# Kernel tuning notes

Hardware: AMD Instinct MI355X
Metric: run time of the kernel (lower is better)

## Reference

```python
import jax, jax.numpy as jnp
import numpy as np
from jax import lax

C, H, W = 1024, 128, 128
N = 4096
SIZE_RATIO = 8.0
ITERS = 10
INIT_LAMBDA = 0.01
MIN_LAMBDA = 1e-6
MAX_LAMBDA = 100.0


def to_homogeneous(x):
    return jnp.concatenate([x, jnp.ones(x.shape[:-1] + (1,), x.dtype)], -1)


def from_homogeneous(x):
    return x[..., :-1] / x[..., -1:]


def skew_symmetric(v):  # [..., 3] -> [..., 3, 3]
    x, y, z = v[..., 0], v[..., 1], v[..., 2]
    o = jnp.zeros_like(x)
    return jnp.stack([
        jnp.stack([o, -z, y], -1),
        jnp.stack([z, o, -x], -1),
        jnp.stack([-y, x, o], -1)], -2)


def so3exp_map(w):  # [3] -> [3, 3], Rodrigues with small-angle guard
    theta2 = jnp.sum(w * w)
    theta = jnp.sqrt(jnp.maximum(theta2, 1e-24))
    A = jnp.where(theta2 < 1e-16, 1.0, jnp.sin(theta) / theta)
    B = jnp.where(theta2 < 1e-16, 0.5, (1.0 - jnp.cos(theta)) / jnp.maximum(theta2, 1e-24))
    K = skew_symmetric(w)
    return jnp.eye(3, dtype=w.dtype) + A * K + B * (K @ K)


def sobel_filter(img):  # img [C,H,W] -> (gx, gy), depthwise 3x3 sobel (normalized /8)
    c = img.shape[0]
    kx = jnp.asarray(np.array([[-1, 0, 1], [-2, 0, 2], [-1, 0, 1]], np.float32) / 8.0)
    ky = kx.T
    def dw(k):
        kern = jnp.tile(k[None, None], (c, 1, 1, 1))  # [C,1,3,3]
        return lax.conv_general_dilated(img[None], kern, (1, 1), 'SAME',
                                        feature_group_count=c,
                                        dimension_numbers=('NCHW', 'OIHW', 'NCHW'))[0]
    return dw(kx), dw(ky)


def bilinear_interpolation(img, idx):  # img [C,H,W], idx [N,2] = (x, y); returns [N,C]
    _, h, w = img.shape
    x, y = idx[:, 0], idx[:, 1]
    x0 = jnp.floor(x)
    y0 = jnp.floor(y)
    wx = x - x0
    wy = y - y0
    x0i = jnp.clip(x0.astype(jnp.int32), 0, w - 1)
    x1i = jnp.clip(x0i + 1, 0, w - 1)
    y0i = jnp.clip(y0.astype(jnp.int32), 0, h - 1)
    y1i = jnp.clip(y0i + 1, 0, h - 1)
    f00 = img[:, y0i, x0i]  # [C,N]
    f10 = img[:, y0i, x1i]
    f01 = img[:, y1i, x0i]
    f11 = img[:, y1i, x1i]
    out = (f00 * (1 - wx) * (1 - wy) + f10 * wx * (1 - wy)
           + f01 * (1 - wx) * wy + f11 * wx * wy)
    return out.T  # [N,C]


def _np_rodrigues(axis, angle):
    axis = np.asarray(axis, np.float64)
    axis = axis / np.linalg.norm(axis)
    K = np.array([[0, -axis[2], axis[1]], [axis[2], 0, -axis[0]], [-axis[1], axis[0], 0]])
    return (np.eye(3) + np.sin(angle) * K + (1 - np.cos(angle)) * (K @ K)).astype(np.float32)


def setup_inputs() -> dict:
    rng = np.random.default_rng(0)
    imgf0 = jnp.asarray(rng.standard_normal((C, H, W)).astype(np.float32))
    imgf1 = jnp.asarray(rng.standard_normal((C, H, W)).astype(np.float32))
    pts3d = np.stack([rng.uniform(-1.2, 1.2, N), rng.uniform(-1.2, 1.2, N),
                      rng.uniform(4.0, 8.0, N)], -1).astype(np.float32)
    K = np.array([[1200.0, 0.0, 512.0], [0.0, 1200.0, 512.0], [0.0, 0.0, 1.0]], np.float32)
    proj = pts3d @ K.T
    pts2d = (proj[:, :2] / proj[:, 2:3]).astype(np.float32)
    r_matrix = np.eye(4, dtype=np.float32)  # reference pose
    q_matrix = np.eye(4, dtype=np.float32)  # query pose: small rotation + translation
    q_matrix[:3, :3] = _np_rodrigues([0.3, 0.5, 0.8], 0.02)
    q_matrix[:3, 3] = np.array([0.05, -0.03, 0.02], np.float32)
    return {
        'imgf0': imgf0, 'imgf1': imgf1,
        'points_2D': jnp.asarray(pts2d), 'points_3D': jnp.asarray(pts3d),
        'q_matrix': jnp.asarray(q_matrix), 'r_matrix': jnp.asarray(r_matrix),
        'K1': jnp.asarray(K),
    }


def reference(imgf0, imgf1, points_2D, points_3D, q_matrix, r_matrix, K1):
    # --- setup (matches FeaturePnP.forward preamble) ---
    r_inv = jnp.linalg.inv(r_matrix)
    relative = q_matrix @ r_inv
    R_init = relative[:3, :3]
    t_init = relative[:3, 3]
    gx, gy = sobel_filter(imgf1)
    feat0 = bilinear_interpolation(imgf0, points_2D / SIZE_RATIO)  # [N,C]
    pts3d0 = from_homogeneous(to_homogeneous(points_3D) @ r_matrix.T)  # [N,3]
    fx, fy = K1[0, 0], K1[1, 1]
    eye3 = jnp.broadcast_to(jnp.eye(3, dtype=points_3D.dtype), (N, 3, 3))
    wmax = jnp.float32(W - 1)
    hmax = jnp.float32(H - 1)

    def project(R, t):
        p3 = pts3d0 @ R.T + t                      # [N,3]
        p2 = from_homogeneous(p3 @ K1.T)           # [N,2]
        idx = p2 / SIZE_RATIO
        idx = jnp.stack([jnp.clip(idx[:, 0], 0.0, wmax),
                         jnp.clip(idx[:, 1], 0.0, hmax)], -1)
        return p3, p2, idx

    def cost_at(idx):
        feat1 = bilinear_interpolation(imgf1, idx)
        err = feat1 - feat0
        return err, jnp.mean(jnp.sum(err * err, -1))

    _, pts2d_init, idx_init = project(R_init, t_init)
    _, cost_init = cost_at(idx_init)

    def step(state, _):
        R, t, lam, prev_cost, best = state
        p3, _, idx = project(R, t)
        feat1 = bilinear_interpolation(imgf1, idx)
        error = feat1 - feat0                       # [N,C]
        # Jacobians (squared_loss -> weights = 1)
        J_p_T = jnp.concatenate([eye3, -skew_symmetric(p3)], -1)  # [N,3,6]
        z = p3[:, 2]
        o = jnp.ones_like(z)
        zr = jnp.zeros_like(z)
        J_h_p = jnp.stack([o * fx, zr, -fx * p3[:, 0] / z,
                           zr, o * fy, -fy * p3[:, 1] / z], -1).reshape(N, 2, 3)
        J_h_p = J_h_p / z[:, None, None] / SIZE_RATIO
        Jex = bilinear_interpolation(gx, idx)       # [N,C]
        Jey = bilinear_interpolation(gy, idx)
        J_e_h = jnp.stack([Jex, Jey], -1)           # [N,C,2]
        J = jnp.matmul(jnp.matmul(J_e_h, J_h_p), J_p_T)  # [N,C,6]
        g = jnp.einsum('nck,nc->k', J, error)       # [6]
        Hs = jnp.einsum('nck,ncl->kl', J, J)        # [6,6]
        Hd = Hs + jnp.diag(jnp.diagonal(Hs) + 1e-9) * lam
        delta = -jnp.linalg.solve(Hd, g)
        dt, dw = delta[:3], delta[3:6]
        dr = so3exp_map(dw)
        R_new = dr @ R
        t_new = dr @ t + dt
        _, new_p2, new_idx = project(R_new, t_new)
        _, new_cost = cost_at(new_idx)
        accept = new_cost <= prev_cost
        R2 = jnp.where(accept, R_new, R)
        t2 = jnp.where(accept, t_new, t)
        best2 = jnp.where(accept, new_p2, best)
        prev2 = jnp.where(accept, new_cost, prev_cost)
        lam2 = jnp.clip(lam * jnp.where(accept, 0.1, 10.0), MIN_LAMBDA, MAX_LAMBDA)
        return (R2, t2, lam2, prev2, best2), None

    init_state = (R_init, t_init, jnp.float32(INIT_LAMBDA), cost_init, pts2d_init)
    (_, _, _, _, best_pts_2d), _ = lax.scan(step, init_state, None, length=ITERS)
    return best_pts_2d
```

## Files before the change

### kernel.cpp

```cpp
#include <hip/hip_runtime.h>
#include <math.h>

#define NPTS 4096
#define NCH  1024
#define HH 128
#define WW 128
#define SLICE (HH*WW)
#define PARTW 2048
#define NBLK  2048

struct WsPtrs {
  double* Hg;
  float* state;
  float* p3d0;
  float* idx0x;
  float* idx0y;
  float* nidxx;
  float* nidxy;
  float* np2;
  float* best;
  float* P12;
  float* part;
  float* feat0;
  float* feat0t;
  float* img1t;
};

__device__ inline float w3f(int k){ return (k==1)?2.f:((k==0||k==2)?1.f:0.f); }
__device__ inline float d3f(int k){ return (k==0)?-0.125f:((k==2)?0.125f:0.f); }

__device__ void lm_solve_commit(int force, WsPtrs& ws, const double* stot, int* sacc)
{
  float cost_new = (float)(stot[27] / (double)NPTS);
  int acc = force || (cost_new <= ws.state[13]);
  if (acc){
    ws.state[13]=cost_new;
    for (int k=0;k<9;k++) ws.state[k]=ws.state[14+k];
    for (int k=0;k<3;k++) ws.state[9+k]=ws.state[23+k];
    for (int a=0;a<27;a++) ws.Hg[a]=stot[a];
  }
  if (!force){
    float l = ws.state[12]*(acc?0.1f:10.f);
    ws.state[12]=fminf(fmaxf(l,1e-6f),100.f);
  }
  *sacc=acc;
  double M[6][7];
  {
    double Hf[6][6]; int p=0;
    for (int k=0;k<6;k++) for (int l=k;l<6;l++){ double v=ws.Hg[p++]; Hf[k][l]=v; Hf[l][k]=v; }
    double lam = (double)ws.state[12];
    for (int k=0;k<6;k++){
      for (int l=0;l<6;l++) M[k][l]=Hf[k][l];
      M[k][6]=ws.Hg[21+k];
    }
    for (int k=0;k<6;k++) M[k][k] = M[k][k] + (M[k][k] + 1e-9)*lam;
  }
  for (int k=0;k<6;k++){
    int pi=k; double bv=fabs(M[k][k]);
    for (int i=k+1;i<6;i++){ double v=fabs(M[i][k]); if(v>bv){bv=v;pi=i;} }
    if (pi!=k) for (int j=k;j<7;j++){ double tmp=M[k][j];M[k][j]=M[pi][j];M[pi][j]=tmp; }
    double pv=M[k][k];
    for (int i=k+1;i<6;i++){
      double f2=M[i][k]/pv;
      for (int j=k;j<7;j++) M[i][j]-=f2*M[k][j];
    }
  }
  double x[6];
  for (int k=5;k>=0;k--){
    double s=M[k][6];
    for (int j=k+1;j<6;j++) s-=M[k][j]*x[j];
    x[k]=s/M[k][k];
  }
  float dt0=(float)(-x[0]), dt1=(float)(-x[1]), dt2=(float)(-x[2]);
  float w0=(float)(-x[3]), w1=(float)(-x[4]), w2=(float)(-x[5]);
  float th2 = w0*w0+w1*w1+w2*w2;
  float th = sqrtf(fmaxf(th2, 1e-24f));
  float A_ = (th2 < 1e-16f) ? 1.f : (sinf(th)/th);
  float B_ = (th2 < 1e-16f) ? 0.5f : ((1.f - cosf(th)) / fmaxf(th2, 1e-24f));
  float Kx[9] = {0.f,-w2,w1,  w2,0.f,-w0,  -w1,w0,0.f};
  float K2[9];
  for (int i=0;i<3;i++) for (int j=0;j<3;j++){
    float s=0.f; for (int k=0;k<3;k++) s+=Kx[i*3+k]*Kx[k*3+j];
    K2[i*3+j]=s;
  }
  float dr[9];
  for (int i=0;i<9;i++) dr[i] = ((i%4==0)?1.f:0.f) + A_*Kx[i] + B_*K2[i];
  float Rn[9], tn[3];
  for (int i=0;i<3;i++) for (int j=0;j<3;j++){
    float s=0.f; for (int k=0;k<3;k++) s+=dr[i*3+k]*ws.state[k*3+j];
    Rn[i*3+j]=s;
  }
  for (int i=0;i<3;i++){
    float s=0.f; for (int k=0;k<3;k++) s+=dr[i*3+k]*ws.state[9+k];
    tn[i]=s+((i==0)?dt0:(i==1)?dt1:dt2);
  }
  for (int k=0;k<9;k++) ws.state[14+k]=Rn[k];
  for (int k=0;k<3;k++) ws.state[23+k]=tn[k];
}

__global__ __launch_bounds__(256) void prep_init_kernel(
    const float* __restrict__ pts2d, const float* __restrict__ pts3d,
    const float* __restrict__ qm, const float* __restrict__ rm,
    const float* __restrict__ K1, WsPtrs ws)
{
  const int t = threadIdx.x;
  if (t == 0) {
    double M[4][8];
    for (int i=0;i<4;i++) for (int j=0;j<4;j++){ M[i][j]=rm[i*4+j]; M[i][4+j]=(i==j)?1.0:0.0; }
    for (int k=0;k<4;k++){
      int p=k; double bv=fabs(M[k][k]);
      for (int i=k+1;i<4;i++){ double v=fabs(M[i][k]); if(v>bv){bv=v;p=i;} }
      if (p!=k) for (int j=0;j<8;j++){ double tmp=M[k][j]; M[k][j]=M[p][j]; M[p][j]=tmp; }
      double pv = M[k][k];
      for (int j=0;j<8;j++) M[k][j] /= pv;
      for (int i=0;i<4;i++) if (i!=k){
        double f2=M[i][k];
        for (int j=0;j<8;j++) M[i][j] -= f2*M[k][j];
      }
    }
    float rel[16];
    for (int i=0;i<4;i++) for (int j=0;j<4;j++){
      float s=0.f;
      for (int k=0;k<4;k++) s += qm[i*4+k]*(float)M[k][4+j];
      rel[i*4+j]=s;
    }
    for (int i=0;i<3;i++) for (int j=0;j<3;j++){ ws.state[i*3+j]=rel[i*4+j]; ws.state[14+i*3+j]=rel[i*4+j]; }
    for (int i=0;i<3;i++){ ws.state[9+i]=rel[i*4+3]; ws.state[23+i]=rel[i*4+3]; }
    ws.state[12] = 0.01f;
  }
  for (int i=0;i<16;i++){
    int n = t + i*256;
    float X=pts3d[n*3+0], Y=pts3d[n*3+1], Z=pts3d[n*3+2];
    float hx = rm[0]*X + rm[1]*Y + rm[2]*Z + rm[3];
    float hy = rm[4]*X + rm[5]*Y + rm[6]*Z + rm[7];
    float hz = rm[8]*X + rm[9]*Y + rm[10]*Z + rm[11];
    float hw = rm[12]*X + rm[13]*Y + rm[14]*Z + rm[15];
    ws.p3d0[n]=hx/hw; ws.p3d0[NPTS+n]=hy/hw; ws.p3d0[2*NPTS+n]=hz/hw;
    ws.idx0x[n]=pts2d[n*2+0]*0.125f;
    ws.idx0y[n]=pts2d[n*2+1]*0.125f;
  }
}

__global__ __launch_bounds__(256) void feat0_kernel(
    const float* __restrict__ img0, const float* __restrict__ pts2d, WsPtrs ws)
{
  __shared__ __align__(16) float tile[SLICE];
  const int c = blockIdx.x;
  const int t = threadIdx.x;
  {
    const float4* g4 = reinterpret_cast<const float4*>(img0 + (size_t)c*SLICE);
    float4* t4 = reinterpret_cast<float4*>(tile);
    #pragma unroll
    for (int i=0;i<16;i++) t4[t + i*256] = g4[t + i*256];
  }
  __syncthreads();
  #pragma unroll
  for (int i=0;i<16;i++){
    int n = t + i*256;
    float x = pts2d[n*2+0]*0.125f, y = pts2d[n*2+1]*0.125f;
    float x0f=floorf(x), y0f=floorf(y);
    float wx=x-x0f, wy=y-y0f;
    int xi=min(max((int)x0f,0),WW-1);
    int yi=min(max((int)y0f,0),HH-1);
    int x1=min(xi+1,WW-1), y1=min(yi+1,HH-1);
    float f00=tile[yi*WW+xi], f10=tile[yi*WW+x1], f01=tile[y1*WW+xi], f11=tile[y1*WW+x1];
    ws.feat0[(size_t)c*NPTS + n] =
      f00*(1.f-wx)*(1.f-wy) + f10*wx*(1.f-wy) + f01*(1.f-wx)*wy + f11*wx*wy;
  }
}

__global__ __launch_bounds__(256) void transpose_kernel(
    const float* __restrict__ src, float* __restrict__ dst, int R, int Cc)
{
  __shared__ float tile[32][33];
  int bx = blockIdx.x*32, by = blockIdx.y*32;
  int tx = threadIdx.x & 31, ty = threadIdx.x >> 5;
  #pragma unroll
  for (int k=0;k<4;k++){
    int r = by + ty + k*8;
    tile[ty + k*8][tx] = src[(size_t)r*Cc + bx + tx];
  }
  __syncthreads();
  #pragma unroll
  for (int k=0;k<4;k++){
    int r = bx + ty + k*8;
    dst[(size_t)r*R + by + tx] = tile[tx][ty + k*8];
  }
}

__global__ __launch_bounds__(256) void iter_score_kernel(
    const float* __restrict__ img1t, const float* __restrict__ f0t,
    const float* __restrict__ K1, WsPtrs ws)
{
  __shared__ float4 scoef[2][16];
  __shared__ float sr[2][12];
  __shared__ float red6[4][6];
  __shared__ float sh6[6];
  const int b = blockIdx.x, t = threadIdx.x;
  const int n0 = b*2;

  if (t < 32){
    const int pt = t>>4, p = t&15;
    const int n = n0 + pt;
    const float fx=K1[0], cx=K1[2], fy=K1[4], cy=K1[5];
    float sRt[12];
    #pragma unroll
    for (int k=0;k<12;k++) sRt[k]=ws.state[14+k];
    float px=ws.p3d0[n], py=ws.p3d0[NPTS+n], pz=ws.p3d0[2*NPTS+n];
    float X = sRt[0]*px + sRt[1]*py + sRt[2]*pz + sRt[9];
    float Y = sRt[3]*px + sRt[4]*py + sRt[5]*pz + sRt[10];
    float Z = sRt[6]*px + sRt[7]*py + sRt[8]*pz + sRt[11];
    float p2x = (fx*X + cx*Z)/Z;
    float p2y = (fy*Y + cy*Z)/Z;
    float xx = fminf(fmaxf(p2x*0.125f,0.f),(float)(WW-1));
    float yy = fminf(fmaxf(p2y*0.125f,0.f),(float)(HH-1));
    float a = (fx/Z)*0.125f;
    float bb = (fy/Z)*0.125f;
    float c = ((-fx*X)/Z)/Z*0.125f;
    float d = ((-fy*Y)/Z)/Z*0.125f;
    if (p == 0){
      ws.np2[2*n]=p2x; ws.np2[2*n+1]=p2y;
      sr[pt][0]=a;  sr[pt][1]=0.f; sr[pt][2]=c;  sr[pt][3]=c*Y;       sr[pt][4]=a*Z-c*X; sr[pt][5]=-a*Y;
      sr[pt][6]=0.f; sr[pt][7]=bb; sr[pt][8]=d;  sr[pt][9]=d*Y-bb*Z;  sr[pt][10]=-d*X;   sr[pt][11]=bb*X;
    }
    float x0f=floorf(xx), y0f=floorf(yy);
    float wx=xx-x0f, wy=yy-y0f;
    int xi=(int)x0f, yi=(int)y0f;
    int x1c=min(xi+1,WW-1), y1c=min(yi+1,HH-1);
    int c1 = x1c-(xi-1);
    int rr1 = y1c-(yi-1);
    float w00=(1.f-wx)*(1.f-wy), w10=wx*(1.f-wy), w01=(1.f-wx)*wy, w11=wx*wy;
    const int r = p>>2, cc = p&3;
    float a1r=w3f(r), d1r=d3f(r);
    int k2=r-rr1+1;
    float a2r=w3f(k2), d2r=d3f(k2);
    float e1r=(r==1)?1.f:0.f, e2r=(r==rr1)?1.f:0.f;
    int sy=yi-1+r;
    bool iny=(sy>=0)&&(sy<HH);
    int ay=min(max(sy,0),HH-1);
    float a1c=w3f(cc), d1c=d3f(cc);
    int k2c=cc-c1+1;
    float a2c=w3f(k2c), d2c=d3f(k2c);
    float e1c=(cc==1)?1.f:0.f, e2c=(cc==c1)?1.f:0.f;
    int sx=xi-1+cc;
    bool inb = iny && (sx>=0) && (sx<WW);
    int ax=min(max(sx,0),WW-1);
    float wf  = e1r*(w00*e1c + w10*e2c) + e2r*(w01*e1c + w11*e2c);
    float wgx = inb ? (a1r*(w00*d1c + w10*d2c) + a2r*(w01*d1c + w11*d2c)) : 0.f;
    float wgy = inb ? (d1r*(w00*a1c + w10*a2c) + d2r*(w01*a1c + w11*a2c)) : 0.f;
    float4 cf; cf.x=wf; cf.y=wgx; cf.z=wgy; cf.w=__int_as_float(ay*WW+ax);
    scoef[pt][p]=cf;
  }
  int kk=0, ll=0;
  if (t < 21){ int rem=t, k=0; while (rem >= 6-k){ rem -= 6-k; k++; } kk=k; ll=k+rem; }
  __syncthreads();

  float part28 = 0.f;
  const float* ip = img1t + 4*t;
  #pragma unroll
  for (int pt=0; pt<2; pt++){
    float f10=0.f,f11=0.f,f12=0.f,f13=0.f;
    float gx0=0.f,gx1=0.f,gx2=0.f,gx3=0.f;
    float gy0=0.f,gy1=0.f,gy2=0.f,gy3=0.f;
    #pragma unroll
    for (int p=0;p<16;p++){
      float4 cf = scoef[pt][p];
      int pix = __float_as_int(cf.w);
      float4 v = *(const float4*)(ip + ((size_t)pix<<10));
      f10 = fmaf(cf.x, v.x, f10); f11 = fmaf(cf.x, v.y, f11);
      f12 = fmaf(cf.x, v.z, f12); f13 = fmaf(cf.x, v.w, f13);
      gx0 = fmaf(cf.y, v.x, gx0); gx1 = fmaf(cf.y, v.y, gx1);
      gx2 = fmaf(cf.y, v.z, gx2); gx3 = fmaf(cf.y, v.w, gx3);
      gy0 = fmaf(cf.z, v.x, gy0); gy1 = fmaf(cf.z, v.y, gy1);
      gy2 = fmaf(cf.z, v.z, gy2); gy3 = fmaf(cf.z, v.w, gy3);
    }
    float4 f0 = *(const float4*)(f0t + ((size_t)(n0+pt)<<10) + 4*t);
    float e0=f10-f0.x, e1=f11-f0.y, e2=f12-f0.z, e3=f13-f0.w;
    float v6[6];
    v6[0] = gx0*gx0 + gx1*gx1 + gx2*gx2 + gx3*gx3;
    v6[1] = gx0*gy0 + gx1*gy1 + gx2*gy2 + gx3*gy3;
    v6[2] = gy0*gy0 + gy1*gy1 + gy2*gy2 + gy3*gy3;
    v6[3] = e0*gx0 + e1*gx1 + e2*gx2 + e3*gx3;
    v6[4] = e0*gy0 + e1*gy1 + e2*gy2 + e3*gy3;
    v6[5] = e0*e0 + e1*e1 + e2*e2 + e3*e3;
    #pragma unroll
    for (int j=0;j<6;j++){
      float vv=v6[j];
      for (int off=32; off>0; off>>=1) vv += __shfl_down(vv, off, 64);
      v6[j]=vv;
    }
    int wave=t>>6, lane=t&63;
    if (lane==0){
      #pragma unroll
      for (int j=0;j<6;j++) red6[wave][j]=v6[j];
    }
    __syncthreads();
    if (t<6) sh6[t] = red6[0][t]+red6[1][t]+red6[2][t]+red6[3][t];
    __syncthreads();
    if (t<28){
      float m0=sh6[0], m1=sh6[1], m2=sh6[2], s0=sh6[3], s1=sh6[4], ss=sh6[5];
      const float* r0 = sr[pt];
      const float* r1 = sr[pt]+6;
      float ev;
      if (t<21)      ev = m0*r0[kk]*r0[ll] + m1*(r0[kk]*r1[ll] + r1[kk]*r0[ll]) + m2*r1[kk]*r1[ll];
      else if (t<27) ev = s0*r0[t-21] + s1*r1[t-21];
      else           ev = ss;
      part28 += ev;
    }
    __syncthreads();
  }
  if (t<28) ws.part[(size_t)t*PARTW + b] = part28;
}

__global__ __launch_bounds__(256) void solve_kernel(
    int force, WsPtrs ws, float* __restrict__ dout)
{
  const int t = threadIdx.x;
  __shared__ float red[4*28];
  __shared__ double stot[28];
  __shared__ int sacc;
  float loc[28];
  #pragma unroll
  for (int a=0;a<28;a++){
    const float* pa = ws.part + (size_t)a*PARTW;
    float s=0.f;
    #pragma unroll
    for (int k=0;k<8;k++) s += pa[t + k*256];
    loc[a]=s;
  }
  #pragma unroll
  for (int a=0;a<28;a++){
    float vv=loc[a];
    for (int off=32;off>0;off>>=1) vv += __shfl_down(vv,off,64);
    loc[a]=vv;
  }
  int wave=t>>6, lane=t&63;
  if (lane==0){
    #pragma unroll
    for (int a=0;a<28;a++) red[wave*28+a]=loc[a];
  }
  __syncthreads();
  if (t<28) stot[t] = (double)red[t]+(double)red[28+t]+(double)red[56+t]+(double)red[84+t];
  __syncthreads();
  if (t==0) lm_solve_commit(force, ws, stot, &sacc);
  __syncthreads();
  int acc=sacc;
  float2* best2=(float2*)ws.best;
  const float2* np22=(const float2*)ws.np2;
  float2* out2=(float2*)dout;
  #pragma unroll
  for (int i=0;i<16;i++){
    int n=t+i*256;
    if (acc) best2[n]=np22[n];
    out2[n]=best2[n];
  }
}


__global__ __launch_bounds__(256) void build_kernel(const float* __restrict__ K1, WsPtrs ws)
{
  const int n = blockIdx.x*256 + threadIdx.x;
  const float fx=K1[0], cx=K1[2], fy=K1[4], cy=K1[5];
  float sRt[12];
  #pragma unroll
  for (int k=0;k<12;k++) sRt[k]=ws.state[14+k];
  float px=ws.p3d0[n], py=ws.p3d0[NPTS+n], pz=ws.p3d0[2*NPTS+n];
  float X = sRt[0]*px + sRt[1]*py + sRt[2]*pz + sRt[9];
  float Y = sRt[3]*px + sRt[4]*py + sRt[5]*pz + sRt[10];
  float Z = sRt[6]*px + sRt[7]*py + sRt[8]*pz + sRt[11];
  float p2x = (fx*X + cx*Z)/Z;
  float p2y = (fy*Y + cy*Z)/Z;
  ws.np2[2*n]=p2x; ws.np2[2*n+1]=p2y;
  float xx = fminf(fmaxf(p2x*0.125f,0.f),(float)(WW-1));
  float yy = fminf(fmaxf(p2y*0.125f,0.f),(float)(HH-1));
  ws.nidxx[n]=xx; ws.nidxy[n]=yy;
  float a = (fx/Z)*0.125f;
  float b = (fy/Z)*0.125f;
  float c = ((-fx*X)/Z)/Z*0.125f;
  float d = ((-fy*Y)/Z)/Z*0.125f;
  float r0[6] = {a, 0.f, c, c*Y, a*Z - c*X, -a*Y};
  float r1[6] = {0.f, b, d, d*Y - b*Z, -d*X, b*X};
  #pragma unroll
  for (int k=0;k<6;k++){ ws.P12[n*12+k]=r0[k]; ws.P12[n*12+6+k]=r1[k]; }
}

__global__ __launch_bounds__(256) void bigfb_kernel(
    const float* __restrict__ img0, const float* __restrict__ img1, WsPtrs ws)
{
  __shared__ __align__(16) float tile[SLICE];
  const int c = blockIdx.x;
  const int t = threadIdx.x;
  {
    const float4* g4 = reinterpret_cast<const float4*>(img1 + (size_t)c*SLICE);
    float4* t4 = reinterpret_cast<float4*>(tile);
    #pragma unroll
    for (int i=0;i<16;i++) t4[t + i*256] = g4[t + i*256];
  }
  __syncthreads();
  float f1a[16], gxa[16], gya[16];
  #pragma unroll
  for (int i=0;i<16;i++){
    int n = t + i*256;
    float x = ws.nidxx[n], y = ws.nidxy[n];
    float x0f = floorf(x), y0f = floorf(y);
    float wx = x - x0f, wy = y - y0f;
    int xi = (int)x0f, yi = (int)y0f;
    float v[4][4];
    if (xi>=1 && xi<=WW-3 && yi>=1 && yi<=HH-3) {
      int base = (yi-1)*WW + (xi-1);
      #pragma unroll
      for (int r=0;r<4;r++)
        #pragma unroll
        for (int cc=0;cc<4;cc++)
          v[r][cc] = tile[base + r*WW + cc];
    } else {
      #pragma unroll
      for (int r=0;r<4;r++){
        int ry = yi-1+r;
        bool okr = (ry>=0) && (ry<HH);
        int ryc = min(max(ry,0),HH-1);
        #pragma unroll
        for (int cc=0;cc<4;cc++){
          int rx = xi-1+cc;
          bool ok = okr && (rx>=0) && (rx<WW);
          int rxc = min(max(rx,0),WW-1);
          float val = tile[ryc*WW + rxc];
          v[r][cc] = ok ? val : 0.f;
        }
      }
    }
    float D1[4], D2[4], E0a[4], E1a[4];
    #pragma unroll
    for (int r=0;r<4;r++){ D1[r]=v[r][2]-v[r][0]; D2[r]=v[r][3]-v[r][1]; }
    #pragma unroll
    for (int cc=0;cc<4;cc++){ E0a[cc]=v[2][cc]-v[0][cc]; E1a[cc]=v[3][cc]-v[1][cc]; }
    float gx00 = D1[0] + 2.f*D1[1] + D1[2];
    float gx01 = D2[0] + 2.f*D2[1] + D2[2];
    float gx10 = D1[1] + 2.f*D1[2] + D1[3];
    float gx11 = D2[1] + 2.f*D2[2] + D2[3];
    float gy00 = E0a[0] + 2.f*E0a[1] + E0a[2];
    float gy01 = E0a[1] + 2.f*E0a[2] + E0a[3];
    float gy10 = E1a[0] + 2.f*E1a[1] + E1a[2];
    float gy11 = E1a[1] + 2.f*E1a[2] + E1a[3];
    float w00=(1.f-wx)*(1.f-wy), w10=wx*(1.f-wy), w01=(1.f-wx)*wy, w11=wx*wy;
    f1a[i] = w00*v[1][1] + w10*v[1][2] + w01*v[2][1] + w11*v[2][2];
    gxa[i] = 0.125f*(w00*gx00 + w10*gx01 + w01*gx10 + w11*gx11);
    gya[i] = 0.125f*(w00*gy00 + w10*gy01 + w01*gy10 + w11*gy11);
  }
  __syncthreads();
  {
    const float4* g4 = reinterpret_cast<const float4*>(img0 + (size_t)c*SLICE);
    float4* t4 = reinterpret_cast<float4*>(tile);
    #pragma unroll
    for (int i=0;i<16;i++) t4[t + i*256] = g4[t + i*256];
  }
  __syncthreads();
  float acc[28];
  #pragma unroll
  for (int a=0;a<28;a++) acc[a]=0.f;
  for (int i=0;i<16;i++){
    int n = t + i*256;
    float x = ws.idx0x[n], y = ws.idx0y[n];
    float x0f=floorf(x), y0f=floorf(y);
    float wx=x-x0f, wy=y-y0f;
    int xi=min(max((int)x0f,0),WW-1);
    int yi=min(max((int)y0f,0),HH-1);
    int x1=min(xi+1,WW-1), y1=min(yi+1,HH-1);
    float f00=tile[yi*WW+xi], f10=tile[yi*WW+x1], f01=tile[y1*WW+xi], f11=tile[y1*WW+x1];
    float feat0 = f00*(1.f-wx)*(1.f-wy) + f10*wx*(1.f-wy) + f01*(1.f-wx)*wy + f11*wx*wy;
    float e = f1a[i] - feat0;
    float gx = gxa[i], gy = gya[i];
    const float* r0 = ws.P12 + (size_t)n*12;
    const float* r1 = r0 + 6;
    float jv[6];
    #pragma unroll
    for (int k=0;k<6;k++) jv[k] = gx*r0[k] + gy*r1[k];
    int p=0;
    #pragma unroll
    for (int k=0;k<6;k++)
      #pragma unroll
      for (int l=k;l<6;l++)
        { acc[p] += jv[k]*jv[l]; p++; }
    #pragma unroll
    for (int k=0;k<6;k++) acc[21+k] += e*jv[k];
    acc[27] += e*e;
  }
  __syncthreads();
  #pragma unroll
  for (int a=0;a<28;a++){
    float vv=acc[a];
    for (int off=32; off>0; off>>=1) vv += __shfl_down(vv, off, 64);
    acc[a]=vv;
  }
  int wave = t>>6, lane = t&63;
  if (lane==0){
    #pragma unroll
    for (int a=0;a<28;a++) tile[wave*28+a]=acc[a];
  }
  __syncthreads();
  if (t<28){
    float s = tile[t]+tile[28+t]+tile[56+t]+tile[84+t];
    ws.part[(size_t)t*PARTW + c] = s;
    ws.part[(size_t)t*PARTW + 1024 + c] = 0.f;
  }
}

extern "C" void kernel_launch(void* const* d_in, const int* in_sizes, int n_in,
                              void* d_out, int out_size, void* d_ws, size_t ws_size,
                              hipStream_t stream) {
  (void)in_sizes; (void)n_in; (void)out_size;
  const float* img0  = (const float*)d_in[0];
  const float* img1  = (const float*)d_in[1];
  const float* pts2d = (const float*)d_in[2];
  const float* pts3d = (const float*)d_in[3];
  const float* qm    = (const float*)d_in[4];
  const float* rm    = (const float*)d_in[5];
  const float* K1    = (const float*)d_in[6];
  float* out = (float*)d_out;

  char* w = (char*)d_ws;
  WsPtrs ws;
  ws.Hg      = (double*)w;
  ws.state   = (float*)(w + 256);
  float* f = (float*)(w + 512);
  ws.p3d0  = f; f += 3*NPTS;
  ws.idx0x = f; f += NPTS;
  ws.idx0y = f; f += NPTS;
  ws.nidxx = f; f += NPTS;
  ws.nidxy = f; f += NPTS;
  ws.np2   = f; f += 2*NPTS;
  ws.best  = f; f += 2*NPTS;
  ws.P12   = f; f += 12*NPTS;
  ws.part  = f; f += 28*PARTW;
  ws.feat0  = f; f += (size_t)NCH*NPTS;
  ws.feat0t = f; f += (size_t)NCH*NPTS;
  ws.img1t  = f; f += (size_t)NCH*SLICE;
  size_t need = ((char*)f) - w;
  bool fast = (ws_size >= need);

  prep_init_kernel<<<1,256,0,stream>>>(pts2d, pts3d, qm, rm, K1, ws);
  if (fast) {
    feat0_kernel<<<NCH,256,0,stream>>>(img0, pts2d, ws);
    transpose_kernel<<<dim3(NPTS/32, NCH/32),256,0,stream>>>(ws.feat0, ws.feat0t, NCH, NPTS);
    transpose_kernel<<<dim3(SLICE/32, NCH/32),256,0,stream>>>(img1, ws.img1t, NCH, SLICE);
    iter_score_kernel<<<NBLK,256,0,stream>>>(ws.img1t, ws.feat0t, K1, ws);
    solve_kernel<<<1,256,0,stream>>>(1, ws, out);
    for (int it=0; it<10; ++it){
      iter_score_kernel<<<NBLK,256,0,stream>>>(ws.img1t, ws.feat0t, K1, ws);
      solve_kernel<<<1,256,0,stream>>>(0, ws, out);
    }
  } else {
    build_kernel<<<NPTS/256,256,0,stream>>>(K1, ws);
    bigfb_kernel<<<NCH,256,0,stream>>>(img0, img1, ws);
    solve_kernel<<<1,256,0,stream>>>(1, ws, out);
    for (int it=0; it<10; ++it){
      build_kernel<<<NPTS/256,256,0,stream>>>(K1, ws);
      bigfb_kernel<<<NCH,256,0,stream>>>(img0, img1, ws);
      solve_kernel<<<1,256,0,stream>>>(0, ws, out);
    }
  }
}
```

Measured before the change: 769.6 us.

## Store transposed image and features as bf16 and process both points concurrently

The transpose kernels now convert the channel-last copies of img1 and feat0 to packed bf16, which halves the bytes gathered per iteration in the score kernel. The score kernel is restructured so each half of the block handles one of the two points with 8 channels per thread, instead of looping over the points with barriers in between. This cuts the dominant gather traffic and the synchronisation, at the cost of bf16 rounding in the image and reference features feeding the LM cost and Hessian.

```diff
diff --git a/kernel.cpp b/kernel.cpp
--- a/kernel.cpp
+++ b/kernel.cpp
@@ -29,6 +29,18 @@
 __device__ inline float w3f(int k){ return (k==1)?2.f:((k==0||k==2)?1.f:0.f); }
 __device__ inline float d3f(int k){ return (k==0)?-0.125f:((k==2)?0.125f:0.f); }
 
+__device__ inline unsigned int f2bf(float f){
+  unsigned int u = __float_as_uint(f);
+  unsigned int r = u + 0x7fffu + ((u>>16)&1u);
+  return r>>16;
+}
+__device__ inline void unpack8(uint4 v, float* f){
+  f[0]=__uint_as_float(v.x<<16); f[1]=__uint_as_float(v.x&0xffff0000u);
+  f[2]=__uint_as_float(v.y<<16); f[3]=__uint_as_float(v.y&0xffff0000u);
+  f[4]=__uint_as_float(v.z<<16); f[5]=__uint_as_float(v.z&0xffff0000u);
+  f[6]=__uint_as_float(v.w<<16); f[7]=__uint_as_float(v.w&0xffff0000u);
+}
+
 __device__ void lm_solve_commit(int force, WsPtrs& ws, const double* stot, int* sacc)
 {
   float cost_new = (float)(stot[27] / (double)NPTS);
@@ -169,33 +181,35 @@
   }
 }
 
-__global__ __launch_bounds__(256) void transpose_kernel(
-    const float* __restrict__ src, float* __restrict__ dst, int R, int Cc)
-{
-  __shared__ float tile[32][33];
-  int bx = blockIdx.x*32, by = blockIdx.y*32;
-  int tx = threadIdx.x & 31, ty = threadIdx.x >> 5;
+__global__ __launch_bounds__(256) void cvt_transpose_kernel(
+    const float* __restrict__ src, unsigned int* __restrict__ dst, int R, int Cc)
+{
+  __shared__ float tile[64][33];
+  const int bx = blockIdx.x*32, by = blockIdx.y*64;
+  const int tx = threadIdx.x & 31, ty = threadIdx.x >> 5;
+  #pragma unroll
+  for (int k=0;k<8;k++){
+    int ch = ty + k*8;
+    tile[ch][tx] = src[(size_t)(by+ch)*Cc + bx + tx];
+  }
+  __syncthreads();
+  const int halfR = R>>1;
   #pragma unroll
   for (int k=0;k<4;k++){
-    int r = by + ty + k*8;
-    tile[ty + k*8][tx] = src[(size_t)r*Cc + bx + tx];
-  }
-  __syncthreads();
-  #pragma unroll
-  for (int k=0;k<4;k++){
-    int r = bx + ty + k*8;
-    dst[(size_t)r*R + by + tx] = tile[tx][ty + k*8];
+    int pix = ty + k*8;
+    float a = tile[2*tx][pix], b = tile[2*tx+1][pix];
+    dst[(size_t)(bx+pix)*halfR + (by>>1) + tx] = f2bf(a) | (f2bf(b)<<16);
   }
 }
 
 __global__ __launch_bounds__(256) void iter_score_kernel(
-    const float* __restrict__ img1t, const float* __restrict__ f0t,
+    const unsigned int* __restrict__ img1t, const unsigned int* __restrict__ f0t,
     const float* __restrict__ K1, WsPtrs ws)
 {
   __shared__ float4 scoef[2][16];
   __shared__ float sr[2][12];
   __shared__ float red6[4][6];
-  __shared__ float sh6[6];
+  __shared__ float sh12[12];
   const int b = blockIdx.x, t = threadIdx.x;
   const int n0 = b*2;
 
@@ -255,61 +269,68 @@
   if (t < 21){ int rem=t, k=0; while (rem >= 6-k){ rem -= 6-k; k++; } kk=k; ll=k+rem; }
   __syncthreads();
 
-  float part28 = 0.f;
-  const float* ip = img1t + 4*t;
-  #pragma unroll
-  for (int pt=0; pt<2; pt++){
-    float f10=0.f,f11=0.f,f12=0.f,f13=0.f;
-    float gx0=0.f,gx1=0.f,gx2=0.f,gx3=0.f;
-    float gy0=0.f,gy1=0.f,gy2=0.f,gy3=0.f;
-    #pragma unroll
-    for (int p=0;p<16;p++){
-      float4 cf = scoef[pt][p];
-      int pix = __float_as_int(cf.w);
-      float4 v = *(const float4*)(ip + ((size_t)pix<<10));
-      f10 = fmaf(cf.x, v.x, f10); f11 = fmaf(cf.x, v.y, f11);
-      f12 = fmaf(cf.x, v.z, f12); f13 = fmaf(cf.x, v.w, f13);
-      gx0 = fmaf(cf.y, v.x, gx0); gx1 = fmaf(cf.y, v.y, gx1);
-      gx2 = fmaf(cf.y, v.z, gx2); gx3 = fmaf(cf.y, v.w, gx3);
-      gy0 = fmaf(cf.z, v.x, gy0); gy1 = fmaf(cf.z, v.y, gy1);
-      gy2 = fmaf(cf.z, v.z, gy2); gy3 = fmaf(cf.z, v.w, gy3);
-    }
-    float4 f0 = *(const float4*)(f0t + ((size_t)(n0+pt)<<10) + 4*t);
-    float e0=f10-f0.x, e1=f11-f0.y, e2=f12-f0.z, e3=f13-f0.w;
-    float v6[6];
-    v6[0] = gx0*gx0 + gx1*gx1 + gx2*gx2 + gx3*gx3;
-    v6[1] = gx0*gy0 + gx1*gy1 + gx2*gy2 + gx3*gy3;
-    v6[2] = gy0*gy0 + gy1*gy1 + gy2*gy2 + gy3*gy3;
-    v6[3] = e0*gx0 + e1*gx1 + e2*gx2 + e3*gx3;
-    v6[4] = e0*gy0 + e1*gy1 + e2*gy2 + e3*gy3;
-    v6[5] = e0*e0 + e1*e1 + e2*e2 + e3*e3;
-    #pragma unroll
-    for (int j=0;j<6;j++){
-      float vv=v6[j];
-      for (int off=32; off>0; off>>=1) vv += __shfl_down(vv, off, 64);
-      v6[j]=vv;
-    }
-    int wave=t>>6, lane=t&63;
-    if (lane==0){
-      #pragma unroll
-      for (int j=0;j<6;j++) red6[wave][j]=v6[j];
-    }
-    __syncthreads();
-    if (t<6) sh6[t] = red6[0][t]+red6[1][t]+red6[2][t]+red6[3][t];
-    __syncthreads();
-    if (t<28){
-      float m0=sh6[0], m1=sh6[1], m2=sh6[2], s0=sh6[3], s1=sh6[4], ss=sh6[5];
-      const float* r0 = sr[pt];
-      const float* r1 = sr[pt]+6;
-      float ev;
-      if (t<21)      ev = m0*r0[kk]*r0[ll] + m1*(r0[kk]*r1[ll] + r1[kk]*r0[ll]) + m2*r1[kk]*r1[ll];
-      else if (t<27) ev = s0*r0[t-21] + s1*r1[t-21];
-      else           ev = ss;
-      part28 += ev;
-    }
-    __syncthreads();
-  }
-  if (t<28) ws.part[(size_t)t*PARTW + b] = part28;
+  const int pt = t>>7, lt = t&127;
+  const int n = n0 + pt;
+  const uint4* ip = (const uint4*)img1t;
+  float f1[8], gx[8], gy[8];
+  #pragma unroll
+  for (int j=0;j<8;j++){ f1[j]=0.f; gx[j]=0.f; gy[j]=0.f; }
+  #pragma unroll
+  for (int p=0;p<16;p++){
+    float4 cf = scoef[pt][p];
+    int pix = __float_as_int(cf.w);
+    uint4 v = ip[(size_t)pix*128 + lt];
+    float vf[8]; unpack8(v, vf);
+    #pragma unroll
+    for (int j=0;j<8;j++){
+      f1[j] = fmaf(cf.x, vf[j], f1[j]);
+      gx[j] = fmaf(cf.y, vf[j], gx[j]);
+      gy[j] = fmaf(cf.z, vf[j], gy[j]);
+    }
+  }
+  uint4 f0v = ((const uint4*)f0t)[(size_t)n*128 + lt];
+  float f0f[8]; unpack8(f0v, f0f);
+  float v6[6] = {0.f,0.f,0.f,0.f,0.f,0.f};
+  #pragma unroll
+  for (int j=0;j<8;j++){
+    float e = f1[j]-f0f[j];
+    v6[0] = fmaf(gx[j],gx[j],v6[0]);
+    v6[1] = fmaf(gx[j],gy[j],v6[1]);
+    v6[2] = fmaf(gy[j],gy[j],v6[2]);
+    v6[3] = fmaf(e,gx[j],v6[3]);
+    v6[4] = fmaf(e,gy[j],v6[4]);
+    v6[5] = fmaf(e,e,v6[5]);
+  }
+  #pragma unroll
+  for (int j=0;j<6;j++){
+    float vv=v6[j];
+    for (int off=32; off>0; off>>=1) vv += __shfl_down(vv, off, 64);
+    v6[j]=vv;
+  }
+  int wave=t>>6, lane=t&63;
+  if (lane==0){
+    #pragma unroll
+    for (int j=0;j<6;j++) red6[wave][j]=v6[j];
+  }
+  __syncthreads();
+  if (t<12) sh12[t] = red6[(t/6)*2][t%6] + red6[(t/6)*2+1][t%6];
+  __syncthreads();
+  if (t<28){
+    float ev = 0.f;
+    #pragma unroll
+    for (int q=0;q<2;q++){
+      float m0=sh12[q*6+0], m1=sh12[q*6+1], m2=sh12[q*6+2];
+      float s0=sh12[q*6+3], s1=sh12[q*6+4], ss=sh12[q*6+5];
+      const float* r0 = sr[q];
+      const float* r1 = sr[q]+6;
+      float e2;
+      if (t<21)      e2 = m0*r0[kk]*r0[ll] + m1*(r0[kk]*r1[ll] + r1[kk]*r0[ll]) + m2*r1[kk]*r1[ll];
+      else if (t<27) e2 = s0*r0[t-21] + s1*r1[t-21];
+      else           e2 = ss;
+      ev += e2;
+    }
+    ws.part[(size_t)t*PARTW + b] = ev;
+  }
 }
 
 __global__ __launch_bounds__(256) void solve_kernel(
@@ -533,20 +554,24 @@
   ws.P12   = f; f += 12*NPTS;
   ws.part  = f; f += 28*PARTW;
   ws.feat0  = f; f += (size_t)NCH*NPTS;
-  ws.feat0t = f; f += (size_t)NCH*NPTS;
-  ws.img1t  = f; f += (size_t)NCH*SLICE;
+  ws.feat0t = f; f += (size_t)NCH*NPTS/2;
+  ws.img1t  = f; f += (size_t)NCH*SLICE/2;
   size_t need = ((char*)f) - w;
   bool fast = (ws_size >= need);
 
   prep_init_kernel<<<1,256,0,stream>>>(pts2d, pts3d, qm, rm, K1, ws);
   if (fast) {
     feat0_kernel<<<NCH,256,0,stream>>>(img0, pts2d, ws);
-    transpose_kernel<<<dim3(NPTS/32, NCH/32),256,0,stream>>>(ws.feat0, ws.feat0t, NCH, NPTS);
-    transpose_kernel<<<dim3(SLICE/32, NCH/32),256,0,stream>>>(img1, ws.img1t, NCH, SLICE);
-    iter_score_kernel<<<NBLK,256,0,stream>>>(ws.img1t, ws.feat0t, K1, ws);
+    cvt_transpose_kernel<<<dim3(NPTS/32, NCH/64),256,0,stream>>>(
+        ws.feat0, (unsigned int*)ws.feat0t, NCH, NPTS);
+    cvt_transpose_kernel<<<dim3(SLICE/32, NCH/64),256,0,stream>>>(
+        img1, (unsigned int*)ws.img1t, NCH, SLICE);
+    iter_score_kernel<<<NBLK,256,0,stream>>>(
+        (const unsigned int*)ws.img1t, (const unsigned int*)ws.feat0t, K1, ws);
     solve_kernel<<<1,256,0,stream>>>(1, ws, out);
     for (int it=0; it<10; ++it){
-      iter_score_kernel<<<NBLK,256,0,stream>>>(ws.img1t, ws.feat0t, K1, ws);
+      iter_score_kernel<<<NBLK,256,0,stream>>>(
+          (const unsigned int*)ws.img1t, (const unsigned int*)ws.feat0t, K1, ws);
       solve_kernel<<<1,256,0,stream>>>(0, ws, out);
     }
   } else {
```

Measured after the change: 772.2 us. About the same (+0.3%).
